# Performance work log

Hardware: AMD Instinct MI355X
Metric: run time of the kernel (lower is better)

The kernel has to match this reference:

```python
import jax, jax.numpy as jnp
import numpy as np

N = 10000
E = 160000
IN_DIM = 128
OUT_DIM = 32
HEADS = 32
H1 = OUT_DIM * 2   # 64 per-head channels in layer 1
H2 = OUT_DIM       # 32 per-head channels in layer 2
NEG_SLOPE = 0.2
EPS = 1e-16  # PyG softmax denominator epsilon


def gat_layer(x, src, dst, W, a_src, a_dst, b, n_nodes, heads, ch):
    # x: [N, F_in], W: [F_in, heads*ch], a_src/a_dst: [heads, ch], b: [ch]
    xp = (x @ W).reshape(n_nodes, heads, ch)                 # [N,H,C]
    alpha_s = jnp.einsum('nhc,hc->nh', xp, a_src)            # [N,H]
    alpha_d = jnp.einsum('nhc,hc->nh', xp, a_dst)            # [N,H]
    e = jax.nn.leaky_relu(alpha_s[src] + alpha_d[dst], NEG_SLOPE)  # [E,H]
    # segment softmax over edges grouped by destination node
    m = jax.ops.segment_max(e, dst, num_segments=n_nodes)    # [N,H]
    e = jnp.exp(e - m[dst])                                  # [E,H]
    s = jax.ops.segment_sum(e, dst, num_segments=n_nodes)    # [N,H]
    alpha = e / (s[dst] + EPS)                               # [E,H]
    msg = alpha[:, :, None] * xp[src]                        # [E,H,C]
    out = jax.ops.segment_sum(msg, dst, num_segments=n_nodes)  # [N,H,C]
    return out.mean(axis=1) + b                              # concat=False: head mean, [N,C]


def setup_inputs() -> dict:
    key = jax.random.key(0)
    ks = jax.random.split(key, 9)
    x = jax.random.normal(ks[0], (N, IN_DIM), dtype=jnp.float32)
    edge_index = jax.random.randint(ks[1], (2, E), 0, N, dtype=jnp.int64)
    W1 = jax.random.normal(ks[2], (IN_DIM, HEADS * H1), dtype=jnp.float32) * 0.1
    a_src1 = jax.random.normal(ks[3], (HEADS, H1), dtype=jnp.float32) * 0.1
    a_dst1 = jax.random.normal(ks[4], (HEADS, H1), dtype=jnp.float32) * 0.1
    b1 = jnp.zeros((H1,), dtype=jnp.float32)
    W2 = jax.random.normal(ks[5], (H1, HEADS * H2), dtype=jnp.float32) * 0.1
    a_src2 = jax.random.normal(ks[6], (HEADS, H2), dtype=jnp.float32) * 0.1
    a_dst2 = jax.random.normal(ks[7], (HEADS, H2), dtype=jnp.float32) * 0.1
    b2 = jnp.zeros((H2,), dtype=jnp.float32)
    return {"x": x, "edge_index": edge_index,
            "W1": W1, "a_src1": a_src1, "a_dst1": a_dst1, "b1": b1,
            "W2": W2, "a_src2": a_src2, "a_dst2": a_dst2, "b2": b2}


def reference(x, edge_index, W1, a_src1, a_dst1, b1, W2, a_src2, a_dst2, b2):
    # flow='source_to_target': messages go edge_index[0] -> edge_index[1]
    src = edge_index[0]
    dst = edge_index[1]
    z1 = jax.nn.elu(gat_layer(x, src, dst, W1, a_src1, a_dst1, b1, N, HEADS, H1))
    z2 = jax.nn.elu(gat_layer(z1, src, dst, W2, a_src2, a_dst2, b2, N, HEADS, H2))
    return jnp.concatenate((z1, z2), axis=-1)  # [N, 96]
```

## Files before the change

### kernel.cpp

```cpp
#include <hip/hip_runtime.h>
#include <hip/hip_bf16.h>

#define NN 10000
#define NE 160000
#define NH 32
#define LRELU_SLOPE 0.2f
#define SM_EPS 1e-16f
#define SM_SHIFT 16.0f

typedef __hip_bfloat16 bf16;
typedef __attribute__((ext_vector_type(8))) __bf16 bf16x8;
typedef __attribute__((ext_vector_type(4))) float f32x4;

__device__ __forceinline__ float asf(unsigned int u) {
    union { unsigned int u; float f; } v; v.u = u; return v.f;
}

__global__ void k_detect_zero(const unsigned int* __restrict__ raw, int* __restrict__ flag,
                              int* __restrict__ deg) {
    int i = blockIdx.x * blockDim.x + threadIdx.x;
    if (i < NN) deg[i] = 0;
    if (i == 0) {
        int z = 1;
        for (int j = 1; j < 32; j += 2) z &= (raw[j] == 0u);
        *flag = z;
    }
}
__global__ void k_norm_hist(const int* __restrict__ raw, const int* __restrict__ flag,
                            int* __restrict__ srcv, int* __restrict__ dstv, int* __restrict__ deg) {
    int e = blockIdx.x * blockDim.x + threadIdx.x;
    if (e >= NE) return;
    int s, d;
    if (*flag) { s = raw[2 * e]; d = raw[2 * (NE + e)]; }
    else       { s = raw[e];     d = raw[NE + e]; }
    srcv[e] = s; dstv[e] = d;
    atomicAdd(&deg[d], 1);
}
__global__ void k_scan(const int* __restrict__ deg, int* __restrict__ offs, int* __restrict__ cursor) {
    __shared__ int wsum[16], wpre[16];
    __shared__ int base;
    const int tid = threadIdx.x, lane = tid & 63, wid = tid >> 6;
    if (tid == 0) base = 0;
    __syncthreads();
    for (int chunk = 0; chunk < NN; chunk += 1024) {
        int idx = chunk + tid;
        int v = (idx < NN) ? deg[idx] : 0;
        int s = v;
        #pragma unroll
        for (int off = 1; off < 64; off <<= 1) {
            int t = __shfl_up(s, off);
            if (lane >= off) s += t;
        }
        if (lane == 63) wsum[wid] = s;
        __syncthreads();
        if (wid == 0) {
            int ws = (lane < 16) ? wsum[lane] : 0;
            #pragma unroll
            for (int off = 1; off < 16; off <<= 1) {
                int t = __shfl_up(ws, off);
                if (lane >= off) ws += t;
            }
            if (lane < 16) wpre[lane] = ws;
        }
        __syncthreads();
        int wbase = (wid == 0) ? 0 : wpre[wid - 1];
        int excl = base + wbase + s - v;
        if (idx < NN) { offs[idx] = excl; cursor[idx] = excl; }
        int total = wpre[15];
        __syncthreads();
        if (tid == 0) base += total;
        __syncthreads();
    }
    if (tid == 0) offs[NN] = base;
}
__global__ void k_scatter(const int* __restrict__ srcv, const int* __restrict__ dstv,
                          int* __restrict__ cursor, int* __restrict__ srcs) {
    int e = blockIdx.x * blockDim.x + threadIdx.x;
    if (e < NE) {
        int p = atomicAdd(&cursor[dstv[e]], 1);
        srcs[p] = srcv[e];
    }
}

__global__ void k_prep(const float* __restrict__ X, bf16* __restrict__ Xb,
                       const float* __restrict__ W1, bf16* __restrict__ Wt1,
                       const float* __restrict__ W2, bf16* __restrict__ Wt2) {
    int i = blockIdx.x * blockDim.x + threadIdx.x;
    if (i < NN * 128) { Xb[i] = __float2bfloat16(X[i]); return; }
    i -= NN * 128;
    if (i < 128 * 2048) {
        int k = i / 2048, m = i - k * 2048;
        Wt1[(size_t)m * 128 + k] = __float2bfloat16(W1[i]);
        return;
    }
    i -= 128 * 2048;
    if (i < 64 * 1024) {
        int k = i / 1024, m = i - k * 1024;
        Wt2[(size_t)m * 64 + k] = __float2bfloat16(W2[i]);
    }
}

template<int K, int M, int C>
__global__ __launch_bounds__(256) void k_gemm_mfma(
        const bf16* __restrict__ Xb, const bf16* __restrict__ Wt,
        const float* __restrict__ Asrc, const float* __restrict__ Adst,
        bf16* __restrict__ XPB, float* __restrict__ aS, float* __restrict__ aD) {
    constexpr int BM = 64, BN = 128;
    constexpr int KB = K * 2;
    constexpr int NHB = BN / C;
    constexpr int WPH = C / 32;
    __shared__ char lds[(BM + BN) * KB];
    __shared__ float sredS[4][BM], sredD[4][BM];
    char* lA = lds;
    char* lB = lds + BM * KB;

    const int tid = threadIdx.x;
    const int wv = tid >> 6, ln = tid & 63;
    const int lrow = ln & 15, lkb = ln >> 4;
    const int brow = blockIdx.x * BM;
    const int bcol = blockIdx.y * BN;

    #pragma unroll
    for (int c = 0; c < BM * K / 8 / 256; c++) {
        int it = c * 256 + tid;
        int r = it / (K / 8), kc = (it % (K / 8)) * 8;
        int node = brow + r;
        uint4 v = make_uint4(0u, 0u, 0u, 0u);
        if (node < NN) v = *reinterpret_cast<const uint4*>(&Xb[(size_t)node * K + kc]);
        *reinterpret_cast<uint4*>(lA + ((r * KB + kc * 2) ^ ((r & 7) << 4))) = v;
    }
    #pragma unroll
    for (int c = 0; c < BN * K / 8 / 256; c++) {
        int it = c * 256 + tid;
        int r = it / (K / 8), kc = (it % (K / 8)) * 8;
        uint4 v = *reinterpret_cast<const uint4*>(&Wt[(size_t)(bcol + r) * K + kc]);
        *reinterpret_cast<uint4*>(lB + ((r * KB + kc * 2) ^ ((r & 7) << 4))) = v;
    }
    __syncthreads();

    f32x4 acc[4][2];
    #pragma unroll
    for (int mi = 0; mi < 4; mi++)
        #pragma unroll
        for (int nj = 0; nj < 2; nj++) acc[mi][nj] = (f32x4){0.f, 0.f, 0.f, 0.f};

    #pragma unroll
    for (int ks = 0; ks < K / 32; ks++) {
        const int k0 = ks * 32 + lkb * 8;
        bf16x8 af[4], bfr[2];
        #pragma unroll
        for (int mi = 0; mi < 4; mi++) {
            int r = mi * 16 + lrow;
            af[mi] = *reinterpret_cast<const bf16x8*>(lA + ((r * KB + k0 * 2) ^ ((r & 7) << 4)));
        }
        #pragma unroll
        for (int nj = 0; nj < 2; nj++) {
            int r = wv * 32 + nj * 16 + lrow;
            bfr[nj] = *reinterpret_cast<const bf16x8*>(lB + ((r * KB + k0 * 2) ^ ((r & 7) << 4)));
        }
        #pragma unroll
        for (int mi = 0; mi < 4; mi++)
            #pragma unroll
            for (int nj = 0; nj < 2; nj++)
                acc[mi][nj] = __builtin_amdgcn_mfma_f32_16x16x32_bf16(af[mi], bfr[nj], acc[mi][nj], 0, 0, 0);
    }

    float ar0 = Asrc[bcol + wv * 32 + lrow];
    float ar1 = Asrc[bcol + wv * 32 + 16 + lrow];
    float ad0 = Adst[bcol + wv * 32 + lrow];
    float ad1 = Adst[bcol + wv * 32 + 16 + lrow];

    #pragma unroll
    for (int mi = 0; mi < 4; mi++) {
        #pragma unroll
        for (int r = 0; r < 4; r++) {
            int rowl = mi * 16 + lkb * 4 + r;
            int row = brow + rowl;
            if (row < NN) {
                XPB[(size_t)row * M + bcol + wv * 32 + lrow]      = __float2bfloat16(acc[mi][0][r]);
                XPB[(size_t)row * M + bcol + wv * 32 + 16 + lrow] = __float2bfloat16(acc[mi][1][r]);
            }
            float vs = acc[mi][0][r] * ar0 + acc[mi][1][r] * ar1;
            float vd = acc[mi][0][r] * ad0 + acc[mi][1][r] * ad1;
            vs += __shfl_xor(vs, 1); vd += __shfl_xor(vd, 1);
            vs += __shfl_xor(vs, 2); vd += __shfl_xor(vd, 2);
            vs += __shfl_xor(vs, 4); vd += __shfl_xor(vd, 4);
            vs += __shfl_xor(vs, 8); vd += __shfl_xor(vd, 8);
            if (lrow == 0) {
                sredS[wv][rowl] = vs;
                sredD[wv][rowl] = vd;
            }
        }
    }
    __syncthreads();
    if (tid < BM) {
        int node = brow + tid;
        if (node < NN) {
            #pragma unroll
            for (int hb = 0; hb < NHB; hb++) {
                float ss = 0.f, dd = 0.f;
                #pragma unroll
                for (int w = 0; w < WPH; w++) {
                    ss += sredS[hb * WPH + w][tid];
                    dd += sredD[hb * WPH + w][tid];
                }
                int h = bcol / C + hb;
                aS[node * NH + h] = ss;
                aD[node * NH + h] = dd;
            }
        }
    }
}

__global__ __launch_bounds__(256) void k_score(
        const float* __restrict__ aS, const float* __restrict__ aD,
        const int* __restrict__ offs, const int* __restrict__ srcs,
        float* __restrict__ pE, float* __restrict__ rinv) {
    const int wid = threadIdx.x >> 6, lane = threadIdx.x & 63;
    const int node = blockIdx.x * 4 + wid;
    const int h = lane & 31, el = lane >> 5;
    const int beg = offs[node], end = offs[node + 1];
    const float ad = aD[node * NH + h];
    float ssum = 0.f;
    for (int i = beg + el; i < end; i += 2) {
        int s = srcs[i];
        float sc = aS[s * NH + h] + ad;
        sc = (sc >= 0.f) ? sc : LRELU_SLOPE * sc;
        float p = __expf(sc - SM_SHIFT);
        pE[i * NH + h] = p;
        ssum += p;
    }
    ssum += __shfl_xor(ssum, 32);
    if (el == 0) rinv[node * NH + h] = 1.f / (ssum + SM_EPS);
}

template<int C>
__global__ __launch_bounds__(256) void k_agg_slice(
        const bf16* __restrict__ XPB, const float* __restrict__ pE,
        const float* __restrict__ rinv, const int* __restrict__ offs,
        const int* __restrict__ srcs, float* __restrict__ P, int sg0) {
    constexpr int M = NH * C;
    constexpr int HPS = 128 / C;
    constexpr int CGH = C / 8;
    const int sg = sg0 + (blockIdx.x & 7);
    const int wid = threadIdx.x >> 6, lane = threadIdx.x & 63;
    const int node = (blockIdx.x >> 3) * 4 + wid;
    const int cg = lane & 15, el = lane >> 4;
    const int hl = cg / CGH;
    const int h = sg * HPS + hl;
    const int col = sg * 128 + cg * 8;
    const int beg = offs[node], end = offs[node + 1];
    float acc[8];
    #pragma unroll
    for (int j = 0; j < 8; j++) acc[j] = 0.f;
    int i = beg + el;
    int sN = 0; float pN = 0.f;
    if (i < end) { sN = srcs[i]; pN = pE[i * NH + h]; }
    while (i < end) {
        const int s = sN; const float p = pN;
        const int i2 = i + 4;
        if (i2 < end) { sN = srcs[i2]; pN = pE[i2 * NH + h]; }
        uint4 v = *reinterpret_cast<const uint4*>(&XPB[s * M + col]);
        acc[0] = fmaf(p, asf(v.x << 16),          acc[0]);
        acc[1] = fmaf(p, asf(v.x & 0xffff0000u),  acc[1]);
        acc[2] = fmaf(p, asf(v.y << 16),          acc[2]);
        acc[3] = fmaf(p, asf(v.y & 0xffff0000u),  acc[3]);
        acc[4] = fmaf(p, asf(v.z << 16),          acc[4]);
        acc[5] = fmaf(p, asf(v.z & 0xffff0000u),  acc[5]);
        acc[6] = fmaf(p, asf(v.w << 16),          acc[6]);
        acc[7] = fmaf(p, asf(v.w & 0xffff0000u),  acc[7]);
        i = i2;
    }
    #pragma unroll
    for (int j = 0; j < 8; j++) {
        acc[j] += __shfl_xor(acc[j], 16);
        acc[j] += __shfl_xor(acc[j], 32);
    }
    const float r = rinv[node * NH + h];
    #pragma unroll
    for (int j = 0; j < 8; j++) acc[j] *= r;
    #pragma unroll
    for (int j = 0; j < 8; j++) acc[j] += __shfl_xor(acc[j], 8);
    if constexpr (HPS == 4) {
        #pragma unroll
        for (int j = 0; j < 8; j++) acc[j] += __shfl_xor(acc[j], 4);
    }
    if (el == 0 && cg < CGH) {
        float* dst = &P[((size_t)sg * NN + node) * C + cg * 8];
        *reinterpret_cast<float4*>(dst)     = make_float4(acc[0], acc[1], acc[2], acc[3]);
        *reinterpret_cast<float4*>(dst + 4) = make_float4(acc[4], acc[5], acc[6], acc[7]);
    }
}

template<int C, int NS, bool WZ>
__global__ void k_reduce(const float* __restrict__ P, const float* __restrict__ bias,
                         float* __restrict__ out, int col0, bf16* __restrict__ z1b) {
    constexpr int TPN = C / 4;
    const int tid = threadIdx.x;
    const int node = blockIdx.x * (256 / TPN) + tid / TPN;
    const int c = (tid % TPN) * 4;
    if (node >= NN) return;
    float4 s = make_float4(0.f, 0.f, 0.f, 0.f);
    #pragma unroll
    for (int sg = 0; sg < NS; sg++) {
        float4 v = *reinterpret_cast<const float4*>(&P[((size_t)sg * NN + node) * C + c]);
        s.x += v.x; s.y += v.y; s.z += v.z; s.w += v.w;
    }
    float4 b = *reinterpret_cast<const float4*>(&bias[c]);
    s.x = s.x * (1.0f / NH) + b.x;
    s.y = s.y * (1.0f / NH) + b.y;
    s.z = s.z * (1.0f / NH) + b.z;
    s.w = s.w * (1.0f / NH) + b.w;
    s.x = (s.x > 0.f) ? s.x : expm1f(s.x);
    s.y = (s.y > 0.f) ? s.y : expm1f(s.y);
    s.z = (s.z > 0.f) ? s.z : expm1f(s.z);
    s.w = (s.w > 0.f) ? s.w : expm1f(s.w);
    *reinterpret_cast<float4*>(&out[(size_t)node * 96 + col0 + c]) = s;
    if constexpr (WZ) {
        bf16 hx[4] = {__float2bfloat16(s.x), __float2bfloat16(s.y),
                      __float2bfloat16(s.z), __float2bfloat16(s.w)};
        *reinterpret_cast<uint2*>(&z1b[(size_t)node * C + c]) =
            *reinterpret_cast<const uint2*>(hx);
    }
}

extern "C" void kernel_launch(void* const* d_in, const int* in_sizes, int n_in,
                              void* d_out, int out_size, void* d_ws, size_t ws_size,
                              hipStream_t stream) {
    const float* x   = (const float*)d_in[0];
    const int*   ei  = (const int*)d_in[1];
    const float* W1  = (const float*)d_in[2];
    const float* as1 = (const float*)d_in[3];
    const float* ad1 = (const float*)d_in[4];
    const float* b1  = (const float*)d_in[5];
    const float* W2  = (const float*)d_in[6];
    const float* as2 = (const float*)d_in[7];
    const float* ad2 = (const float*)d_in[8];
    const float* b2  = (const float*)d_in[9];
    float* out = (float*)d_out;

    char* w = (char*)d_ws;
    size_t off = 0;
    auto alloc = [&](size_t bytes) -> void* {
        void* p = w + off;
        off = (off + bytes + 255) & ~(size_t)255;
        return p;
    };
    bf16*  xpb    = (bf16*)alloc((size_t)NN * 2048 * 2);
    float* aS     = (float*)alloc((size_t)NN * NH * 4);
    float* aD     = (float*)alloc((size_t)NN * NH * 4);
    float* pE     = (float*)alloc((size_t)NE * NH * 4);
    float* rinv   = (float*)alloc((size_t)NN * NH * 4);
    float* P1     = (float*)alloc((size_t)16 * NN * 64 * 4);
    float* P2     = P1;
    int*   deg    = (int*)alloc((size_t)NN * 4);
    int*   cursor = (int*)alloc((size_t)NN * 4);
    int*   offs   = (int*)alloc((size_t)(NN + 1) * 4);
    int*   srcs   = (int*)alloc((size_t)NE * 4);
    int*   srcv   = (int*)alloc((size_t)NE * 4);
    int*   dstv   = (int*)alloc((size_t)NE * 4);
    bf16*  Xb     = (bf16*)alloc((size_t)NN * 128 * 2);
    bf16*  Wt1    = (bf16*)alloc((size_t)2048 * 128 * 2);
    bf16*  Wt2    = (bf16*)alloc((size_t)1024 * 64 * 2);
    bf16*  z1b    = (bf16*)alloc((size_t)NN * 64 * 2);
    int*   eflag  = (int*)alloc(256);
    (void)ws_size; (void)in_sizes; (void)n_in; (void)out_size;

    k_detect_zero<<<(NN + 255) / 256, 256, 0, stream>>>((const unsigned int*)ei, eflag, deg);
    k_norm_hist<<<NE / 256, 256, 0, stream>>>(ei, eflag, srcv, dstv, deg);
    k_scan<<<1, 1024, 0, stream>>>(deg, offs, cursor);
    k_scatter<<<NE / 256, 256, 0, stream>>>(srcv, dstv, cursor, srcs);

    k_prep<<<(NN * 128 + 128 * 2048 + 64 * 1024 + 255) / 256, 256, 0, stream>>>(
        x, Xb, W1, Wt1, W2, Wt2);

    k_gemm_mfma<128, 2048, 64><<<dim3((NN + 63) / 64, 2048 / 128), 256, 0, stream>>>(
        Xb, Wt1, as1, ad1, xpb, aS, aD);
    k_score<<<NN / 4, 256, 0, stream>>>(aS, aD, offs, srcs, pE, rinv);
    k_agg_slice<64><<<(NN / 4) * 8, 256, 0, stream>>>(xpb, pE, rinv, offs, srcs, P1, 0);
    k_agg_slice<64><<<(NN / 4) * 8, 256, 0, stream>>>(xpb, pE, rinv, offs, srcs, P1, 8);
    k_reduce<64, 16, true><<<NN / 16, 256, 0, stream>>>(P1, b1, out, 0, z1b);

    k_gemm_mfma<64, 1024, 32><<<dim3((NN + 63) / 64, 1024 / 128), 256, 0, stream>>>(
        z1b, Wt2, as2, ad2, xpb, aS, aD);
    k_score<<<NN / 4, 256, 0, stream>>>(aS, aD, offs, srcs, pE, rinv);
    k_agg_slice<32><<<(NN / 4) * 8, 256, 0, stream>>>(xpb, pE, rinv, offs, srcs, P2, 0);
    k_reduce<32, 8, false><<<(NN * 8 + 255) / 256, 256, 0, stream>>>(P2, b2, out, 64, nullptr);
}
```

Baseline: 276.0 us.

## Compute edge scores per edge in head-major layout and fold softmax sum into aggregation

The per-node score kernel becomes a per-edge kernel that uses a sorted destination array recorded during the scatter. It loads full aS/aD rows as float4 and writes probabilities in head-major [H][E] layout. The softmax denominator is no longer stored in a separate rinv pass but accumulated inside the aggregation loop and reduced with shuffles. This removes load imbalance from high-degree nodes in the score kernel and gives contiguous per-head probability reads in aggregation, at the cost of an extra dstp array and redundant denominator sums across slices.

```diff
diff --git a/kernel.cpp b/kernel.cpp
--- a/kernel.cpp
+++ b/kernel.cpp
@@ -74,11 +74,14 @@
     if (tid == 0) offs[NN] = base;
 }
 __global__ void k_scatter(const int* __restrict__ srcv, const int* __restrict__ dstv,
-                          int* __restrict__ cursor, int* __restrict__ srcs) {
+                          int* __restrict__ cursor, int* __restrict__ srcs,
+                          int* __restrict__ dstp) {
     int e = blockIdx.x * blockDim.x + threadIdx.x;
     if (e < NE) {
-        int p = atomicAdd(&cursor[dstv[e]], 1);
+        int d = dstv[e];
+        int p = atomicAdd(&cursor[d], 1);
         srcs[p] = srcv[e];
+        dstp[p] = d;
     }
 }
 
@@ -212,33 +215,37 @@
     }
 }
 
-__global__ __launch_bounds__(256) void k_score(
+__global__ __launch_bounds__(256) void k_score_edge(
         const float* __restrict__ aS, const float* __restrict__ aD,
-        const int* __restrict__ offs, const int* __restrict__ srcs,
-        float* __restrict__ pE, float* __restrict__ rinv) {
-    const int wid = threadIdx.x >> 6, lane = threadIdx.x & 63;
-    const int node = blockIdx.x * 4 + wid;
-    const int h = lane & 31, el = lane >> 5;
-    const int beg = offs[node], end = offs[node + 1];
-    const float ad = aD[node * NH + h];
-    float ssum = 0.f;
-    for (int i = beg + el; i < end; i += 2) {
-        int s = srcs[i];
-        float sc = aS[s * NH + h] + ad;
-        sc = (sc >= 0.f) ? sc : LRELU_SLOPE * sc;
-        float p = __expf(sc - SM_SHIFT);
-        pE[i * NH + h] = p;
-        ssum += p;
-    }
-    ssum += __shfl_xor(ssum, 32);
-    if (el == 0) rinv[node * NH + h] = 1.f / (ssum + SM_EPS);
+        const int* __restrict__ srcs, const int* __restrict__ dstp,
+        float* __restrict__ pEh) {
+    const int i = blockIdx.x * 256 + threadIdx.x;
+    const int s = srcs[i];
+    const int d = dstp[i];
+    const float4* prs = reinterpret_cast<const float4*>(&aS[s * NH]);
+    const float4* prd = reinterpret_cast<const float4*>(&aD[d * NH]);
+    float4 vs[8], vd[8];
+    #pragma unroll
+    for (int j = 0; j < 8; j++) { vs[j] = prs[j]; vd[j] = prd[j]; }
+    #pragma unroll
+    for (int j = 0; j < 8; j++) {
+        float sc, p;
+        sc = vs[j].x + vd[j].x; sc = (sc >= 0.f) ? sc : LRELU_SLOPE * sc;
+        p = __expf(sc - SM_SHIFT); pEh[(size_t)(4 * j + 0) * NE + i] = p;
+        sc = vs[j].y + vd[j].y; sc = (sc >= 0.f) ? sc : LRELU_SLOPE * sc;
+        p = __expf(sc - SM_SHIFT); pEh[(size_t)(4 * j + 1) * NE + i] = p;
+        sc = vs[j].z + vd[j].z; sc = (sc >= 0.f) ? sc : LRELU_SLOPE * sc;
+        p = __expf(sc - SM_SHIFT); pEh[(size_t)(4 * j + 2) * NE + i] = p;
+        sc = vs[j].w + vd[j].w; sc = (sc >= 0.f) ? sc : LRELU_SLOPE * sc;
+        p = __expf(sc - SM_SHIFT); pEh[(size_t)(4 * j + 3) * NE + i] = p;
+    }
 }
 
 template<int C>
 __global__ __launch_bounds__(256) void k_agg_slice(
-        const bf16* __restrict__ XPB, const float* __restrict__ pE,
-        const float* __restrict__ rinv, const int* __restrict__ offs,
-        const int* __restrict__ srcs, float* __restrict__ P, int sg0) {
+        const bf16* __restrict__ XPB, const float* __restrict__ pEh,
+        const int* __restrict__ offs, const int* __restrict__ srcs,
+        float* __restrict__ P, int sg0) {
     constexpr int M = NH * C;
     constexpr int HPS = 128 / C;
     constexpr int CGH = C / 8;
@@ -250,17 +257,20 @@
     const int h = sg * HPS + hl;
     const int col = sg * 128 + cg * 8;
     const int beg = offs[node], end = offs[node + 1];
+    const float* __restrict__ pErow = pEh + (size_t)h * NE;
     float acc[8];
     #pragma unroll
     for (int j = 0; j < 8; j++) acc[j] = 0.f;
+    float ssum = 0.f;
     int i = beg + el;
     int sN = 0; float pN = 0.f;
-    if (i < end) { sN = srcs[i]; pN = pE[i * NH + h]; }
+    if (i < end) { sN = srcs[i]; pN = pErow[i]; }
     while (i < end) {
         const int s = sN; const float p = pN;
         const int i2 = i + 4;
-        if (i2 < end) { sN = srcs[i2]; pN = pE[i2 * NH + h]; }
-        uint4 v = *reinterpret_cast<const uint4*>(&XPB[s * M + col]);
+        if (i2 < end) { sN = srcs[i2]; pN = pErow[i2]; }
+        uint4 v = *reinterpret_cast<const uint4*>(&XPB[(size_t)s * M + col]);
+        ssum += p;
         acc[0] = fmaf(p, asf(v.x << 16),          acc[0]);
         acc[1] = fmaf(p, asf(v.x & 0xffff0000u),  acc[1]);
         acc[2] = fmaf(p, asf(v.y << 16),          acc[2]);
@@ -276,7 +286,9 @@
         acc[j] += __shfl_xor(acc[j], 16);
         acc[j] += __shfl_xor(acc[j], 32);
     }
-    const float r = rinv[node * NH + h];
+    ssum += __shfl_xor(ssum, 16);
+    ssum += __shfl_xor(ssum, 32);
+    const float r = 1.f / (ssum + SM_EPS);
     #pragma unroll
     for (int j = 0; j < 8; j++) acc[j] *= r;
     #pragma unroll
@@ -349,14 +361,14 @@
     bf16*  xpb    = (bf16*)alloc((size_t)NN * 2048 * 2);
     float* aS     = (float*)alloc((size_t)NN * NH * 4);
     float* aD     = (float*)alloc((size_t)NN * NH * 4);
-    float* pE     = (float*)alloc((size_t)NE * NH * 4);
-    float* rinv   = (float*)alloc((size_t)NN * NH * 4);
+    float* pEh    = (float*)alloc((size_t)NH * NE * 4);
     float* P1     = (float*)alloc((size_t)16 * NN * 64 * 4);
     float* P2     = P1;
     int*   deg    = (int*)alloc((size_t)NN * 4);
     int*   cursor = (int*)alloc((size_t)NN * 4);
     int*   offs   = (int*)alloc((size_t)(NN + 1) * 4);
     int*   srcs   = (int*)alloc((size_t)NE * 4);
+    int*   dstp   = (int*)alloc((size_t)NE * 4);
     int*   srcv   = (int*)alloc((size_t)NE * 4);
     int*   dstv   = (int*)alloc((size_t)NE * 4);
     bf16*  Xb     = (bf16*)alloc((size_t)NN * 128 * 2);
@@ -369,21 +381,21 @@
     k_detect_zero<<<(NN + 255) / 256, 256, 0, stream>>>((const unsigned int*)ei, eflag, deg);
     k_norm_hist<<<NE / 256, 256, 0, stream>>>(ei, eflag, srcv, dstv, deg);
     k_scan<<<1, 1024, 0, stream>>>(deg, offs, cursor);
-    k_scatter<<<NE / 256, 256, 0, stream>>>(srcv, dstv, cursor, srcs);
+    k_scatter<<<NE / 256, 256, 0, stream>>>(srcv, dstv, cursor, srcs, dstp);
 
     k_prep<<<(NN * 128 + 128 * 2048 + 64 * 1024 + 255) / 256, 256, 0, stream>>>(
         x, Xb, W1, Wt1, W2, Wt2);
 
     k_gemm_mfma<128, 2048, 64><<<dim3((NN + 63) / 64, 2048 / 128), 256, 0, stream>>>(
         Xb, Wt1, as1, ad1, xpb, aS, aD);
-    k_score<<<NN / 4, 256, 0, stream>>>(aS, aD, offs, srcs, pE, rinv);
-    k_agg_slice<64><<<(NN / 4) * 8, 256, 0, stream>>>(xpb, pE, rinv, offs, srcs, P1, 0);
-    k_agg_slice<64><<<(NN / 4) * 8, 256, 0, stream>>>(xpb, pE, rinv, offs, srcs, P1, 8);
+    k_score_edge<<<NE / 256, 256, 0, stream>>>(aS, aD, srcs, dstp, pEh);
+    k_agg_slice<64><<<(NN / 4) * 8, 256, 0, stream>>>(xpb, pEh, offs, srcs, P1, 0);
+    k_agg_slice<64><<<(NN / 4) * 8, 256, 0, stream>>>(xpb, pEh, offs, srcs, P1, 8);
     k_reduce<64, 16, true><<<NN / 16, 256, 0, stream>>>(P1, b1, out, 0, z1b);
 
     k_gemm_mfma<64, 1024, 32><<<dim3((NN + 63) / 64, 1024 / 128), 256, 0, stream>>>(
         z1b, Wt2, as2, ad2, xpb, aS, aD);
-    k_score<<<NN / 4, 256, 0, stream>>>(aS, aD, offs, srcs, pE, rinv);
-    k_agg_slice<32><<<(NN / 4) * 8, 256, 0, stream>>>(xpb, pE, rinv, offs, srcs, P2, 0);
+    k_score_edge<<<NE / 256, 256, 0, stream>>>(aS, aD, srcs, dstp, pEh);
+    k_agg_slice<32><<<(NN / 4) * 8, 256, 0, stream>>>(xpb, pEh, offs, srcs, P2, 0);
     k_reduce<32, 8, false><<<(NN * 8 + 255) / 256, 256, 0, stream>>>(P2, b2, out, 64, nullptr);
 }
```

New measurement: 237.6 us. 13.9% less time.
